# Optimization experiments

Hardware: AMD Instinct MI355X
Metric: run time of the kernel (lower is better)

## Reference

```python
import jax, jax.numpy as jnp
import numpy as np

SCORE_THRESH = 0.05
IOU_THRESH = 0.5
TOP_K = 1000      # candidates fed to NMS
MAX_DET = 100     # padded output detections


def _build_anchors(H, W):
    """Standard RetinaNet anchors: levels P3..P7, 3 ratios x 3 scales."""
    ratios = np.array([0.5, 1.0, 2.0])
    scales = np.array([2 ** 0, 2 ** (1.0 / 3.0), 2 ** (2.0 / 3.0)])
    all_anchors = []
    for lvl in [3, 4, 5, 6, 7]:
        stride = 2 ** lvl
        base_size = 2 ** (lvl + 2)
        # 9 base anchors centered at origin (ratio-major, scale-minor ordering)
        s = base_size * np.tile(scales, len(ratios))          # [9]
        r = np.repeat(ratios, len(scales))                    # [9]
        areas = s * s
        w = np.sqrt(areas / r)
        h = w * r
        base = np.stack([-w / 2, -h / 2, w / 2, h / 2], axis=1)  # [9,4]
        fh = (H + stride - 1) // stride
        fw = (W + stride - 1) // stride
        sx = (np.arange(fw) + 0.5) * stride
        sy = (np.arange(fh) + 0.5) * stride
        gx, gy = np.meshgrid(sx, sy)
        shifts = np.stack([gx.ravel(), gy.ravel(), gx.ravel(), gy.ravel()], axis=1)  # [fh*fw,4]
        all_anchors.append((shifts[:, None, :] + base[None, :, :]).reshape(-1, 4))
    return np.concatenate(all_anchors, axis=0).astype(np.float32)  # [A,4]


def setup_inputs() -> dict:
    key = jax.random.key(0)
    k1, k2 = jax.random.split(key)
    H = W = 1024
    C = 80
    anchors = jnp.asarray(_build_anchors(H, W))[None]            # [1,A,4]
    A = anchors.shape[1]
    classifications = jax.random.uniform(k1, (1, A, C), dtype=jnp.float32)
    regressions = jax.random.normal(k2, (1, A, 4), dtype=jnp.float32)
    return {"classifications": classifications, "regressions": regressions,
            "anchors": anchors, "img_h": H, "img_w": W}


def _decode_clip(anchors, regressions, img_h, img_w):
    # BBoxTransform with mean 0, std [0.1,0.1,0.2,0.2]
    aw = anchors[..., 2] - anchors[..., 0]
    ah = anchors[..., 3] - anchors[..., 1]
    acx = anchors[..., 0] + 0.5 * aw
    acy = anchors[..., 1] + 0.5 * ah
    dx = regressions[..., 0] * 0.1
    dy = regressions[..., 1] * 0.1
    dw = regressions[..., 2] * 0.2
    dh = regressions[..., 3] * 0.2
    pcx = acx + dx * aw
    pcy = acy + dy * ah
    pw = jnp.exp(dw) * aw
    ph = jnp.exp(dh) * ah
    boxes = jnp.stack([pcx - 0.5 * pw, pcy - 0.5 * ph,
                       pcx + 0.5 * pw, pcy + 0.5 * ph], axis=-1)
    # ClipBoxes
    lo = jnp.zeros(4, boxes.dtype)
    hi = jnp.array([img_w, img_h, img_w, img_h], boxes.dtype)
    return jnp.clip(boxes, lo, hi)  # [1,A,4]


def _nms_keep(boxes, valid):
    """Sequential greedy NMS over score-sorted boxes [K,4]; returns keep mask [K]."""
    K = boxes.shape[0]
    areas = jnp.maximum(boxes[:, 2] - boxes[:, 0], 0) * jnp.maximum(boxes[:, 3] - boxes[:, 1], 0)
    idx = jnp.arange(K)

    def body(i, keep):
        b = boxes[i]
        xx1 = jnp.maximum(b[0], boxes[:, 0])
        yy1 = jnp.maximum(b[1], boxes[:, 1])
        xx2 = jnp.minimum(b[2], boxes[:, 2])
        yy2 = jnp.minimum(b[3], boxes[:, 3])
        inter = jnp.maximum(xx2 - xx1, 0) * jnp.maximum(yy2 - yy1, 0)
        iou = inter / (areas[i] + areas - inter + 1e-8)
        suppress = (iou > IOU_THRESH) & (idx > i)
        return jnp.where(keep[i], keep & ~suppress, keep)

    return jax.lax.fori_loop(0, K, body, valid)


def reference(classifications, regressions, anchors, img_h, img_w):
    boxes = _decode_clip(anchors, regressions, img_h, img_w)       # [1,A,4]
    scores = jnp.max(classifications, axis=2)                      # [1,A]
    # Score threshold: mask out low scores, keep fixed shape (padded NMS)
    s0 = jnp.where(scores[0] > SCORE_THRESH, scores[0], -1.0)      # [A]
    top_scores, top_idx = jax.lax.top_k(s0, TOP_K)                 # sorted desc
    cand_boxes = boxes[0, top_idx]                                 # [K,4]
    keep = _nms_keep(cand_boxes, top_scores > SCORE_THRESH)        # [K]
    final = jnp.where(keep, top_scores, -1.0)
    det_scores, sel = jax.lax.top_k(final, MAX_DET)                # [100]
    det_idx = top_idx[sel]                                         # indices into A
    det_valid = det_scores > SCORE_THRESH
    cls = classifications[0, det_idx]                              # [100,C]
    nms_scores = jnp.where(det_valid, jnp.max(cls, axis=1), 0.0)
    nms_class = jnp.where(det_valid, jnp.argmax(cls, axis=1), -1)
    det_boxes = jnp.where(det_valid[:, None], boxes[0, det_idx], 0.0)
    return (nms_scores, nms_class, det_boxes)
```

## Files before the change

### kernel.cpp

```cpp
#include <hip/hip_runtime.h>
#include <stdint.h>

#define SCORE_THRESH 0.05f
#define IOU_THRESH 0.5f
#define TOP_K 1000
#define MAX_DET 100

#define UBINS 4096
#define NREP 4
#define CAND_CAP 2048
#define NMS_CHUNK 128

typedef unsigned int u32;
typedef unsigned long long u64;

#define OFF_HIST     0
#define OFF_STATE    65536
#define OFF_BAR      66560
#define MEMSET_LEN   82944
#define OFF_CAND     82944
#define OFF_RFLAG    91136
#define OFF_SIDX     95136
#define OFF_SSCORE   99136
#define OFF_CBOX     103136
#define OFF_M        119136
#define OFF_SCORES   247136

#define BAR_STRIDE_U32 1024

__device__ __forceinline__ u32 order_f32(float f) {
    u32 b = __float_as_uint(f);
    return (b & 0x80000000u) ? ~b : (b | 0x80000000u);
}

__device__ __forceinline__ u32 ubin(float s0) {
    float u = 1.0f - s0;
    u32 bin = __float_as_uint(u) >> 18;
    return bin > (UBINS - 1) ? (UBINS - 1) : bin;
}

__device__ __forceinline__ void st_sc(u32* p, u32 v)   { __hip_atomic_store(p, v, __ATOMIC_RELAXED, __HIP_MEMORY_SCOPE_AGENT); }
__device__ __forceinline__ void st_sc(float* p, float v){ __hip_atomic_store(p, v, __ATOMIC_RELAXED, __HIP_MEMORY_SCOPE_AGENT); }
__device__ __forceinline__ void st_sc(u64* p, u64 v)   { __hip_atomic_store(p, v, __ATOMIC_RELAXED, __HIP_MEMORY_SCOPE_AGENT); }
__device__ __forceinline__ u32  ld_sc(u32* p)          { return __hip_atomic_load(p, __ATOMIC_RELAXED, __HIP_MEMORY_SCOPE_AGENT); }

__device__ __forceinline__ void gbar(u32* barr, int k, int b, int G, bool dowait) {
    __syncthreads();
    u32* base = barr + (size_t)k * BAR_STRIDE_U32;
    if (threadIdx.x == 0) {
        asm volatile("s_waitcnt vmcnt(0)" ::: "memory");
        st_sc(&base[b], 1u);
    }
    if (!dowait) return;
    if (b == 0) {
        for (;;) {
            int my = 1;
            for (int i = (int)threadIdx.x; i < G; i += 256) my &= (int)ld_sc(&base[i]);
            if (__syncthreads_and(my)) break;
        }
        if (threadIdx.x == 0) st_sc(&base[512], 1u);
    } else {
        if (threadIdx.x == 0) {
            while (ld_sc(&base[512]) == 0u) __builtin_amdgcn_s_sleep(8);
        }
    }
    __syncthreads();
    asm volatile("" ::: "memory");
}

union ShMem {
    u32 hl[UBINS / 2];
    u32 wtot[4];
    struct { u32 wcnt[4]; u32 wbase[4]; u32 bbase; } cmp;
    struct { u64 ckeys[8]; u32 wpart[4][8]; } rank;
    struct {
        u64 Ml[2 * NMS_CHUNK * 16];
        u64 keepS[16];
        u32 nib[256];
        int act[TOP_K];
        u32 wsum[4];
        int nactS;
        int det[MAX_DET];
    } nms;
};

__global__ void __launch_bounds__(256, 2)
mega(const float* __restrict__ cls, const float* __restrict__ regs,
     const float* __restrict__ anchors, const int* __restrict__ pH,
     const int* __restrict__ pW, int A, int C,
     char* __restrict__ ws, float* __restrict__ out)
{
    __shared__ ShMem sh;
    __shared__ u32 shcut;
    u32*   hist   = (u32*)(ws + OFF_HIST);
    u32*   state  = (u32*)(ws + OFF_STATE);
    u32*   barr   = (u32*)(ws + OFF_BAR);
    u32*   cand   = (u32*)(ws + OFF_CAND);
    u32*   rflag  = (u32*)(ws + OFF_RFLAG);
    u32*   sidx   = (u32*)(ws + OFF_SIDX);
    float* sscore = (float*)(ws + OFF_SSCORE);
    float* cbox   = (float*)(ws + OFF_CBOX);
    u64*   M      = (u64*)(ws + OFF_M);
    float* scores = (float*)(ws + OFF_SCORES);

    const int t = threadIdx.x;
    const int b = blockIdx.x;
    const int G = gridDim.x;
    const int gid = b * 256 + t;
    const int gstride = G * 256;
    const int lane = t & 63, wv = t >> 6;

    if (C == 80) {
        for (int i = t; i < UBINS / 2; i += 256) sh.hl[i] = 0;
        __syncthreads();
        int sub = t & 3;
        int la  = t >> 2;
        int nstrips = (A + 63) >> 6;
        int per = (nstrips + G - 1) / G;
        for (int s = 0; s < per; s++) {
            int a = (b * per + s) * 64 + la;
            float m = -1e30f;
            if (a < A) {
                const float* p = cls + (size_t)a * 80 + sub * 4;
                #pragma unroll
                for (int k2 = 0; k2 < 5; k2++) {
                    float4 v = *(const float4*)(p + k2 * 16);
                    m = fmaxf(m, fmaxf(fmaxf(v.x, v.y), fmaxf(v.z, v.w)));
                }
            }
            m = fmaxf(m, __shfl_xor(m, 1, 64));
            m = fmaxf(m, __shfl_xor(m, 2, 64));
            if (sub == 0 && a < A) {
                float s0 = (m > SCORE_THRESH) ? m : -1.0f;
                st_sc(&scores[a], s0);
                u32 d = ubin(s0);
                atomicAdd(&sh.hl[d >> 1], (d & 1) ? 0x10000u : 1u);
            }
        }
        __syncthreads();
        u32* rep = hist + (size_t)(b & (NREP - 1)) * UBINS;
        for (int i = t; i < UBINS / 2; i += 256) {
            u32 v = sh.hl[i];
            if (v & 0xFFFFu) atomicAdd(&rep[2 * i],     v & 0xFFFFu);
            if (v >> 16)     atomicAdd(&rep[2 * i + 1], v >> 16);
        }
    } else {
        u32* rep = hist + (size_t)(b & (NREP - 1)) * UBINS;
        for (int a = gid; a < A; a += gstride) {
            const float* p = cls + (size_t)a * C;
            float m = -1e30f;
            for (int c = 0; c < C; c++) m = fmaxf(m, p[c]);
            float s0 = (m > SCORE_THRESH) ? m : -1.0f;
            st_sc(&scores[a], s0);
            atomicAdd(&rep[ubin(s0)], 1u);
        }
    }
    gbar(barr, 0, b, G, true);

    {
        if (t == 0) shcut = UBINS - 1;
        u32 cnt[16];
        #pragma unroll
        for (int i = 0; i < 16; i++) cnt[i] = 0;
        const uint4* hp = (const uint4*)hist;
        #pragma unroll
        for (int r = 0; r < NREP; r++) {
            #pragma unroll
            for (int i = 0; i < 4; i++) {
                uint4 v = hp[r * (UBINS / 4) + t * 4 + i];
                cnt[4*i]   += v.x; cnt[4*i+1] += v.y;
                cnt[4*i+2] += v.z; cnt[4*i+3] += v.w;
            }
        }
        u32 s = 0;
        #pragma unroll
        for (int i = 0; i < 16; i++) s += cnt[i];
        u32 x = s;
        for (int off = 1; off < 64; off <<= 1) {
            u32 v = (u32)__shfl_up((int)x, off, 64);
            if (lane >= off) x += v;
        }
        if (lane == 63) sh.wtot[wv] = x;
        __syncthreads();
        u32 below = x - s;
        for (int w = 0; w < wv; w++) below += sh.wtot[w];
        if (below < TOP_K && below + s >= TOP_K) {
            u32 cum = below;
            for (int i = 0; i < 16; i++) {
                cum += cnt[i];
                if (cum >= TOP_K) { shcut = (u32)(t * 16 + i); break; }
            }
        }
        __syncthreads();
    }
    const u32 cutbin = shcut;

    {
        int nr = (A + gstride - 1) / gstride;
        u32 mycnt = 0;
        for (int r = 0; r < nr; r++) {
            int a = gid + r * gstride;
            mycnt += ((a < A) && (ubin(scores[a]) <= cutbin)) ? 1u : 0u;
        }
        u32 wc = mycnt;
        wc += (u32)__shfl_xor((int)wc, 1, 64);
        wc += (u32)__shfl_xor((int)wc, 2, 64);
        wc += (u32)__shfl_xor((int)wc, 4, 64);
        wc += (u32)__shfl_xor((int)wc, 8, 64);
        wc += (u32)__shfl_xor((int)wc, 16, 64);
        wc += (u32)__shfl_xor((int)wc, 32, 64);
        if (lane == 0) sh.cmp.wcnt[wv] = wc;
        __syncthreads();
        if (t == 0) {
            u32 s = 0;
            #pragma unroll
            for (int w = 0; w < 4; w++) { sh.cmp.wbase[w] = s; s += sh.cmp.wcnt[w]; }
            sh.cmp.bbase = s ? atomicAdd(&state[5 * 32], s) : 0u;
        }
        __syncthreads();
        u32 off = sh.cmp.bbase + sh.cmp.wbase[wv];
        for (int r = 0; r < nr; r++) {
            int a = gid + r * gstride;
            bool pass = (a < A) && (ubin(scores[a]) <= cutbin);
            u64 mask = __ballot(pass ? 1 : 0);
            if (pass) {
                u32 pos = off + (u32)__popcll(mask & ((1ull << lane) - 1ull));
                if (pos < CAND_CAP) st_sc(&cand[pos], (u32)a);
            }
            off += (u32)__popcll(mask);
        }
    }
    gbar(barr, 1, b, G, b < CAND_CAP / 8);

    if (b < CAND_CAP / 8) {
        int n = (int)state[5 * 32]; if (n > CAND_CAP) n = CAND_CAP;
        u64 kj[8];
        #pragma unroll
        for (int q = 0; q < 8; q++) {
            int j = t * 8 + q;
            u64 kk = 0ull;
            if (j < n) {
                u32 a = cand[j];
                kk = ((u64)order_f32(scores[a]) << 32) | (u64)(0xFFFFFFFFu - a);
            }
            kj[q] = kk;
        }
        for (int bb = b; bb < CAND_CAP / 8; bb += G) {
            if (t < 8) {
                int c = bb * 8 + t;
                u64 ck = 0ull;
                if (c < n) {
                    u32 a = cand[c];
                    ck = ((u64)order_f32(scores[a]) << 32) | (u64)(0xFFFFFFFFu - a);
                }
                sh.rank.ckeys[t] = ck;
            }
            __syncthreads();
            u64 ck[8];
            #pragma unroll
            for (int q = 0; q < 8; q++) ck[q] = sh.rank.ckeys[q];
            u32 cnt8[8] = {0,0,0,0,0,0,0,0};
            #pragma unroll
            for (int q = 0; q < 8; q++) {
                u64 kq = kj[q];
                #pragma unroll
                for (int q2 = 0; q2 < 8; q2++) cnt8[q2] += (kq > ck[q2]) ? 1u : 0u;
            }
            #pragma unroll
            for (int q2 = 0; q2 < 8; q2++) {
                u32 x = cnt8[q2];
                x += (u32)__shfl_xor((int)x, 1, 64);
                x += (u32)__shfl_xor((int)x, 2, 64);
                x += (u32)__shfl_xor((int)x, 4, 64);
                x += (u32)__shfl_xor((int)x, 8, 64);
                x += (u32)__shfl_xor((int)x, 16, 64);
                x += (u32)__shfl_xor((int)x, 32, 64);
                if (lane == 0) sh.rank.wpart[wv][q2] = x;
            }
            __syncthreads();
            if (t < 8) {
                int c = bb * 8 + t;
                if (c < n) {
                    u32 rank = sh.rank.wpart[0][t] + sh.rank.wpart[1][t]
                             + sh.rank.wpart[2][t] + sh.rank.wpart[3][t];
                    if (rank < TOP_K) {
                        u32 a = cand[c];
                        st_sc(&sidx[rank], a);
                        st_sc(&sscore[rank], scores[a]);
                        float4 an = *(const float4*)(anchors + (size_t)a * 4);
                        float4 rg = *(const float4*)(regs + (size_t)a * 4);
                        float aw = an.z - an.x, ah = an.w - an.y;
                        float acx = an.x + 0.5f * aw, acy = an.y + 0.5f * ah;
                        float pcx = acx + (rg.x * 0.1f) * aw;
                        float pcy = acy + (rg.y * 0.1f) * ah;
                        float pw = expf(rg.z * 0.2f) * aw;
                        float ph = expf(rg.w * 0.2f) * ah;
                        float W = (float)(*pW), H = (float)(*pH);
                        st_sc(&cbox[rank * 4 + 0], fminf(fmaxf(pcx - 0.5f * pw, 0.0f), W));
                        st_sc(&cbox[rank * 4 + 1], fminf(fmaxf(pcy - 0.5f * ph, 0.0f), H));
                        st_sc(&cbox[rank * 4 + 2], fminf(fmaxf(pcx + 0.5f * pw, 0.0f), W));
                        st_sc(&cbox[rank * 4 + 3], fminf(fmaxf(pcy + 0.5f * ph, 0.0f), H));
                    }
                }
            }
            __syncthreads();
        }
    }
    gbar(barr, 2, b, G, b * 4 < TOP_K);

    {
        const float4* B4 = (const float4*)cbox;
        for (int i = b * 4 + wv; i < TOP_K; i += G * 4) {
            float4 bi = B4[i];
            float ai = fmaxf(bi.z - bi.x, 0.0f) * fmaxf(bi.w - bi.y, 0.0f);
            u64 any = 0ull;
            for (int w = 0; w < 16; w++) {
                int j = w * 64 + lane;
                bool sup = false;
                if (j < TOP_K && j > i) {
                    float4 bj = B4[j];
                    float aj = fmaxf(bj.z - bj.x, 0.0f) * fmaxf(bj.w - bj.y, 0.0f);
                    float xx1 = fmaxf(bi.x, bj.x), yy1 = fmaxf(bi.y, bj.y);
                    float xx2 = fminf(bi.z, bj.z), yy2 = fminf(bi.w, bj.w);
                    float inter = fmaxf(xx2 - xx1, 0.0f) * fmaxf(yy2 - yy1, 0.0f);
                    float iou = inter / (ai + aj - inter + 1e-8f);
                    sup = iou > IOU_THRESH;
                }
                u64 mask = __ballot(sup ? 1 : 0);
                if (lane == 0) { st_sc(&M[(size_t)i * 16 + w], mask); any |= mask; }
            }
            if (lane == 0) st_sc(&rflag[i], (any != 0ull) ? 1u : 0u);
        }
    }
    gbar(barr, 3, b, G, b == 0);

    if (b == 0) {
        {
            u32 nb = 0;
            int j0 = 4 * t;
            #pragma unroll
            for (int q = 0; q < 4; q++) {
                int j = j0 + q;
                if (j < TOP_K && sscore[j] > SCORE_THRESH) nb |= (1u << q);
            }
            sh.nms.nib[t] = nb;
        }
        u32 flags = 0; int cnt = 0;
        {
            int r0 = 4 * t;
            #pragma unroll
            for (int q = 0; q < 4; q++) {
                int r = r0 + q;
                if (r < TOP_K && rflag[r]) { flags |= (1u << q); cnt++; }
            }
        }
        int x = cnt;
        for (int off = 1; off < 64; off <<= 1) {
            int v = __shfl_up(x, off, 64);
            if (lane >= off) x += v;
        }
        if (lane == 63) sh.nms.wsum[wv] = (u32)x;
        __syncthreads();
        if (t < 16) {
            u64 w = 0;
            for (int m2 = 0; m2 < 16; m2++)
                w |= ((u64)sh.nms.nib[t * 16 + m2]) << (4 * m2);
            sh.nms.keepS[t] = w;
        }
        int base = 0;
        for (int w = 0; w < wv; w++) base += (int)sh.nms.wsum[w];
        int pos = base + x - cnt;
        {
            int r0 = 4 * t;
            #pragma unroll
            for (int q = 0; q < 4; q++)
                if (flags & (1u << q)) sh.nms.act[pos++] = r0 + q;
        }
        if (t == 0) {
            int na = 0;
            for (int w = 0; w < 4; w++) na += (int)sh.nms.wsum[w];
            sh.nms.nactS = na;
        }
        __syncthreads();
        int nact = sh.nms.nactS;
        int nchunks = (nact + NMS_CHUNK - 1) / NMS_CHUNK;

        if (nchunks > 0) {
            int cn0 = (nact < NMS_CHUNK) ? nact : NMS_CHUNK;
            for (int i = t; i < cn0 * 16; i += 256) {
                int row = sh.nms.act[i >> 4];
                sh.nms.Ml[i] = M[(size_t)row * 16 + (i & 15)];
            }
        }
        __syncthreads();
        u64 kp = (wv == 0 && lane < 16) ? sh.nms.keepS[lane] : 0ull;
        for (int ci = 0; ci < nchunks; ci++) {
            int c0 = ci * NMS_CHUNK;
            int cn = (nact - c0 < NMS_CHUNK) ? (nact - c0) : NMS_CHUNK;
            int cur = (ci & 1) * (NMS_CHUNK * 16);
            if (ci + 1 < nchunks && t >= 64) {
                int c0n = c0 + NMS_CHUNK;
                int cnn = (nact - c0n < NMS_CHUNK) ? (nact - c0n) : NMS_CHUNK;
                int nxt = ((ci + 1) & 1) * (NMS_CHUNK * 16);
                for (int i = t - 64; i < cnn * 16; i += 192) {
                    int row = sh.nms.act[c0n + (i >> 4)];
                    sh.nms.Ml[nxt + i] = M[(size_t)row * 16 + (i & 15)];
                }
            }
            if (wv == 0) {
                u64 mreg = (lane < 16 && cn > 0) ? sh.nms.Ml[cur + lane] : 0ull;
                for (int k = 0; k < cn; k++) {
                    u64 mnx = (lane < 16 && k + 1 < cn)
                            ? sh.nms.Ml[cur + (k + 1) * 16 + lane] : 0ull;
                    int i = sh.nms.act[c0 + k];
                    u64 kw = __shfl(kp, i >> 6, 64);
                    if ((kw >> (i & 63)) & 1ull) kp &= ~mreg;
                    mreg = mnx;
                }
            }
            __syncthreads();
        }
        if (wv == 0 && lane < 16) sh.nms.keepS[lane] = kp;
        __syncthreads();

        if (t == 0) {
            int cnt2 = 0;
            for (int w = 0; w < 16 && cnt2 < MAX_DET; w++) {
                u64 kw = sh.nms.keepS[w];
                while (kw && cnt2 < MAX_DET) {
                    int bbit = __ffsll((unsigned long long)kw) - 1;
                    sh.nms.det[cnt2++] = w * 64 + bbit;
                    kw &= kw - 1;
                }
            }
            for (; cnt2 < MAX_DET; cnt2++) sh.nms.det[cnt2] = -1;
        }
        __syncthreads();
        if (t < MAX_DET) {
            int i = sh.nms.det[t];
            if (i >= 0) {
                u32 a = sidx[i];
                const float* p = cls + (size_t)a * C;
                float best = -1e30f; int bc = 0;
                if (C == 80) {
                    #pragma unroll
                    for (int c4 = 0; c4 < 20; c4++) {
                        float4 v = *(const float4*)(p + c4 * 4);
                        if (v.x > best) { best = v.x; bc = c4 * 4; }
                        if (v.y > best) { best = v.y; bc = c4 * 4 + 1; }
                        if (v.z > best) { best = v.z; bc = c4 * 4 + 2; }
                        if (v.w > best) { best = v.w; bc = c4 * 4 + 3; }
                    }
                } else {
                    best = p[0]; bc = 0;
                    for (int c = 1; c < C; c++) {
                        float v = p[c];
                        if (v > best) { best = v; bc = c; }
                    }
                }
                out[t] = best;
                out[MAX_DET + t] = (float)bc;
                out[2 * MAX_DET + t * 4 + 0] = cbox[i * 4 + 0];
                out[2 * MAX_DET + t * 4 + 1] = cbox[i * 4 + 1];
                out[2 * MAX_DET + t * 4 + 2] = cbox[i * 4 + 2];
                out[2 * MAX_DET + t * 4 + 3] = cbox[i * 4 + 3];
            } else {
                out[t] = 0.0f;
                out[MAX_DET + t] = -1.0f;
                out[2 * MAX_DET + t * 4 + 0] = 0.0f;
                out[2 * MAX_DET + t * 4 + 1] = 0.0f;
                out[2 * MAX_DET + t * 4 + 2] = 0.0f;
                out[2 * MAX_DET + t * 4 + 3] = 0.0f;
            }
        }
    }
}

extern "C" void kernel_launch(void* const* d_in, const int* in_sizes, int n_in,
                              void* d_out, int out_size, void* d_ws, size_t ws_size,
                              hipStream_t stream) {
    (void)n_in; (void)out_size; (void)ws_size;
    const float* cls     = (const float*)d_in[0];
    const float* regs    = (const float*)d_in[1];
    const float* anchors = (const float*)d_in[2];
    const int*   pH      = (const int*)d_in[3];
    const int*   pW      = (const int*)d_in[4];
    int A = in_sizes[1] / 4;
    int C = in_sizes[0] / A;

    static int nCU = 0;
    if (nCU <= 0) {
        int dev = 0;
        hipGetDevice(&dev);
        hipDeviceGetAttribute(&nCU, hipDeviceAttributeMultiprocessorCount, dev);
        if (nCU <= 0) nCU = 256;
    }
    int G = 2 * nCU;
    if (G > 512) G = 512;
    if (G < 8) G = 8;

    char* ws = (char*)d_ws;
    hipMemsetAsync(ws, 0, MEMSET_LEN, stream);
    mega<<<dim3(G), dim3(256), 0, stream>>>(cls, regs, anchors, pH, pW, A, C,
                                            ws, (float*)d_out);
}
```

Baseline: 153.3 us.

## Store packed score keys in candidates, skip lower-triangle IoU, overlap NMS prep

Compaction now writes 64-bit keys (ordered score plus inverted index) into the candidate buffer, so the ranking stage no longer re-gathers scores by index and decodes score and index straight from the key. The IoU mask stage skips words that lie entirely below the diagonal and writes them as zeros instead of computing them. Block 0 is taken out of the IoU work so it can build the score-validity bitmask before the third barrier. This cuts scattered gathers and about half the IoU work, at the cost of doubling the candidate buffer size and shifting the workspace offsets.

```diff
diff --git a/kernel.cpp b/kernel.cpp
--- a/kernel.cpp
+++ b/kernel.cpp
@@ -19,12 +19,12 @@
 #define OFF_BAR      66560
 #define MEMSET_LEN   82944
 #define OFF_CAND     82944
-#define OFF_RFLAG    91136
-#define OFF_SIDX     95136
-#define OFF_SSCORE   99136
-#define OFF_CBOX     103136
-#define OFF_M        119136
-#define OFF_SCORES   247136
+#define OFF_RFLAG    99328
+#define OFF_SIDX     103328
+#define OFF_SSCORE   107328
+#define OFF_CBOX     111328
+#define OFF_M        127328
+#define OFF_SCORES   255328
 
 #define BAR_STRIDE_U32 1024
 
@@ -95,7 +95,7 @@
     u32*   hist   = (u32*)(ws + OFF_HIST);
     u32*   state  = (u32*)(ws + OFF_STATE);
     u32*   barr   = (u32*)(ws + OFF_BAR);
-    u32*   cand   = (u32*)(ws + OFF_CAND);
+    u64*   cand   = (u64*)(ws + OFF_CAND);
     u32*   rflag  = (u32*)(ws + OFF_RFLAG);
     u32*   sidx   = (u32*)(ws + OFF_SIDX);
     float* sscore = (float*)(ws + OFF_SSCORE);
@@ -221,11 +221,15 @@
         u32 off = sh.cmp.bbase + sh.cmp.wbase[wv];
         for (int r = 0; r < nr; r++) {
             int a = gid + r * gstride;
-            bool pass = (a < A) && (ubin(scores[a]) <= cutbin);
+            float s0 = (a < A) ? scores[a] : 0.0f;
+            bool pass = (a < A) && (ubin(s0) <= cutbin);
             u64 mask = __ballot(pass ? 1 : 0);
             if (pass) {
                 u32 pos = off + (u32)__popcll(mask & ((1ull << lane) - 1ull));
-                if (pos < CAND_CAP) st_sc(&cand[pos], (u32)a);
+                if (pos < CAND_CAP) {
+                    u64 key = ((u64)order_f32(s0) << 32) | (u64)(0xFFFFFFFFu - (u32)a);
+                    st_sc(&cand[pos], key);
+                }
             }
             off += (u32)__popcll(mask);
         }
@@ -238,22 +242,12 @@
         #pragma unroll
         for (int q = 0; q < 8; q++) {
             int j = t * 8 + q;
-            u64 kk = 0ull;
-            if (j < n) {
-                u32 a = cand[j];
-                kk = ((u64)order_f32(scores[a]) << 32) | (u64)(0xFFFFFFFFu - a);
-            }
-            kj[q] = kk;
+            kj[q] = (j < n) ? cand[j] : 0ull;
         }
         for (int bb = b; bb < CAND_CAP / 8; bb += G) {
             if (t < 8) {
                 int c = bb * 8 + t;
-                u64 ck = 0ull;
-                if (c < n) {
-                    u32 a = cand[c];
-                    ck = ((u64)order_f32(scores[a]) << 32) | (u64)(0xFFFFFFFFu - a);
-                }
-                sh.rank.ckeys[t] = ck;
+                sh.rank.ckeys[t] = (c < n) ? cand[c] : 0ull;
             }
             __syncthreads();
             u64 ck[8];
@@ -284,9 +278,12 @@
                     u32 rank = sh.rank.wpart[0][t] + sh.rank.wpart[1][t]
                              + sh.rank.wpart[2][t] + sh.rank.wpart[3][t];
                     if (rank < TOP_K) {
-                        u32 a = cand[c];
+                        u64 kk = ck[t];
+                        u32 a = 0xFFFFFFFFu - (u32)(kk & 0xFFFFFFFFull);
+                        u32 hi = (u32)(kk >> 32);
+                        u32 bits = (hi & 0x80000000u) ? (hi & 0x7FFFFFFFu) : ~hi;
                         st_sc(&sidx[rank], a);
-                        st_sc(&sscore[rank], scores[a]);
+                        st_sc(&sscore[rank], __uint_as_float(bits));
                         float4 an = *(const float4*)(anchors + (size_t)a * 4);
                         float4 rg = *(const float4*)(regs + (size_t)a * 4);
                         float aw = an.z - an.x, ah = an.w - an.y;
@@ -306,15 +303,18 @@
             __syncthreads();
         }
     }
-    gbar(barr, 2, b, G, b * 4 < TOP_K);
-
-    {
+    gbar(barr, 2, b, G, b == 0 || (b - 1) * 4 < TOP_K);
+
+    if (b >= 1) {
         const float4* B4 = (const float4*)cbox;
-        for (int i = b * 4 + wv; i < TOP_K; i += G * 4) {
+        for (int i = (b - 1) * 4 + wv; i < TOP_K; i += (G - 1) * 4) {
             float4 bi = B4[i];
             float ai = fmaxf(bi.z - bi.x, 0.0f) * fmaxf(bi.w - bi.y, 0.0f);
             u64 any = 0ull;
-            for (int w = 0; w < 16; w++) {
+            int w0 = i >> 6;
+            if (lane == 0)
+                for (int w = 0; w < w0; w++) st_sc(&M[(size_t)i * 16 + w], 0ull);
+            for (int w = w0; w < 16; w++) {
                 int j = w * 64 + lane;
                 bool sup = false;
                 if (j < TOP_K && j > i) {
@@ -331,35 +331,15 @@
             }
             if (lane == 0) st_sc(&rflag[i], (any != 0ull) ? 1u : 0u);
         }
-    }
-    gbar(barr, 3, b, G, b == 0);
-
-    if (b == 0) {
-        {
-            u32 nb = 0;
-            int j0 = 4 * t;
-            #pragma unroll
-            for (int q = 0; q < 4; q++) {
-                int j = j0 + q;
-                if (j < TOP_K && sscore[j] > SCORE_THRESH) nb |= (1u << q);
-            }
-            sh.nms.nib[t] = nb;
-        }
-        u32 flags = 0; int cnt = 0;
-        {
-            int r0 = 4 * t;
-            #pragma unroll
-            for (int q = 0; q < 4; q++) {
-                int r = r0 + q;
-                if (r < TOP_K && rflag[r]) { flags |= (1u << q); cnt++; }
-            }
-        }
-        int x = cnt;
-        for (int off = 1; off < 64; off <<= 1) {
-            int v = __shfl_up(x, off, 64);
-            if (lane >= off) x += v;
-        }
-        if (lane == 63) sh.nms.wsum[wv] = (u32)x;
+    } else {
+        u32 nb = 0;
+        int j0 = 4 * t;
+        #pragma unroll
+        for (int q = 0; q < 4; q++) {
+            int j = j0 + q;
+            if (j < TOP_K && sscore[j] > SCORE_THRESH) nb |= (1u << q);
+        }
+        sh.nms.nib[t] = nb;
         __syncthreads();
         if (t < 16) {
             u64 w = 0;
@@ -367,6 +347,26 @@
                 w |= ((u64)sh.nms.nib[t * 16 + m2]) << (4 * m2);
             sh.nms.keepS[t] = w;
         }
+    }
+    gbar(barr, 3, b, G, b == 0);
+
+    if (b == 0) {
+        u32 flags = 0; int cnt = 0;
+        {
+            int r0 = 4 * t;
+            #pragma unroll
+            for (int q = 0; q < 4; q++) {
+                int r = r0 + q;
+                if (r < TOP_K && rflag[r]) { flags |= (1u << q); cnt++; }
+            }
+        }
+        int x = cnt;
+        for (int off = 1; off < 64; off <<= 1) {
+            int v = __shfl_up(x, off, 64);
+            if (lane >= off) x += v;
+        }
+        if (lane == 63) sh.nms.wsum[wv] = (u32)x;
+        __syncthreads();
         int base = 0;
         for (int w = 0; w < wv; w++) base += (int)sh.nms.wsum[w];
         int pos = base + x - cnt;
```

New measurement: 149.8 us, median of 2. 1.02x faster.
